# Kernel optimization log

Measured on AMD Instinct MI355X. Metric: run time of the kernel, lower is better.

The kernel has to match this reference:

```python
import jax, jax.numpy as jnp
import numpy as np
import math


def setup_inputs() -> dict:
    key = jax.random.key(0)
    k1, k2, k3 = jax.random.split(key, 3)
    B, H, T, D = 4, 16, 4096, 128
    return {
        "q": jax.random.normal(k1, (B, H, T, D), dtype=jnp.float32),
        "k": jax.random.normal(k2, (B, H, T, D), dtype=jnp.float32),
        "v": jax.random.normal(k3, (B, H, T, D), dtype=jnp.float32),
        "BS": 32,
    }


def _compress(x, block_size):
    # blockwise mean-pool along T: [B,H,T,D] -> [B,H,C,D], C = ceil(T/BS)
    B, H, T, D = x.shape
    C = math.ceil(T / block_size)
    pad = C * block_size - T
    if pad:
        x = jnp.pad(x, ((0, 0), (0, 0), (0, pad), (0, 0)))
    return x.reshape(B, H, C, block_size, D).mean(axis=3)


def reference(q, k, v, BS):
    dk = k.shape[-1]
    k_cmp = _compress(k, BS)  # [B,H,C,D]
    v_cmp = _compress(v, BS)  # [B,H,C,D]
    # scaled dot-product attention over compressed KV
    score = jnp.einsum("bhtd,bhcd->bhtc", q, k_cmp) / math.sqrt(dk)
    score = jax.nn.softmax(score, axis=-1)  # [B,H,T,C]
    out = jnp.einsum("bhtc,bhcd->bhtd", score, v_cmp)  # [B,H,T,D]
    return (out, score)
```

## Files before the change

kernel.cpp:

```cpp
#include <hip/hip_runtime.h>
#include <hip/hip_bf16.h>

typedef __attribute__((ext_vector_type(8))) short short8;
typedef __attribute__((ext_vector_type(4))) float f32x4;

#define B_  4
#define H_  16
#define T_  4096
#define D_  128
#define BS_ 32
#define C_  128
#define BH_ (B_ * H_)

__device__ __forceinline__ int posperm(int x) {
  return (x & ~31) | (((x >> 2) & 3) << 3) | (((x >> 4) & 1) << 2) | (x & 3);
}

__device__ __forceinline__ unsigned short f2bf(float f) {
  __hip_bfloat16 h = __float2bfloat16(f);
  return __builtin_bit_cast(unsigned short, h);
}

__device__ __forceinline__ void gload_lds16(const uint4* g, uint4* l) {
  __builtin_amdgcn_global_load_lds(
      (const __attribute__((address_space(1))) unsigned int*)g,
      (__attribute__((address_space(3))) unsigned int*)l, 16, 0, 0);
}

__global__ __launch_bounds__(256) void compress_kernel(
    const float* __restrict__ k, const float* __restrict__ v,
    unsigned short* __restrict__ kc, unsigned short* __restrict__ vT) {
  int blk = blockIdx.x;
  int bh  = blk >> 4;
  int cg  = blk & 15;
  int cb  = cg * 8 + (threadIdx.x >> 5);
  int l   = threadIdx.x & 31;
  const float* kp = k + ((size_t)bh * T_ + (size_t)cb * BS_) * D_ + 4 * l;
  const float* vp = v + ((size_t)bh * T_ + (size_t)cb * BS_) * D_ + 4 * l;
  float4 ks = {0.f, 0.f, 0.f, 0.f}, vs = {0.f, 0.f, 0.f, 0.f};
#pragma unroll
  for (int j = 0; j < BS_; ++j) {
    float4 a = *(const float4*)(kp + (size_t)j * D_);
    float4 b = *(const float4*)(vp + (size_t)j * D_);
    ks.x += a.x; ks.y += a.y; ks.z += a.z; ks.w += a.w;
    vs.x += b.x; vs.y += b.y; vs.z += b.z; vs.w += b.w;
  }
  const float s = 1.0f / BS_;
  size_t slab = (size_t)bh * (C_ * D_);
  unsigned short kq[4] = {f2bf(ks.x * s), f2bf(ks.y * s), f2bf(ks.z * s), f2bf(ks.w * s)};
  int p0 = posperm(4 * l) ^ ((cb & 7) << 3);
  *(uint2*)&kc[slab + (size_t)cb * D_ + p0] = *(const uint2*)kq;
  float vv[4] = {vs.x * s, vs.y * s, vs.z * s, vs.w * s};
#pragma unroll
  for (int i = 0; i < 4; ++i) {
    int d = 4 * l + i;
    vT[slab + (size_t)d * C_ + (posperm(cb) ^ ((d & 7) << 3))] = f2bf(vv[i]);
  }
}

__global__ __launch_bounds__(256, 4) void attn_kernel(
    const float* __restrict__ q, const unsigned short* __restrict__ kc,
    const unsigned short* __restrict__ vT, float* __restrict__ out,
    float* __restrict__ score) {
  __shared__ uint4 sbuf[2048];

  int blk    = blockIdx.x;
  int bh     = blk >> 6;
  int tchunk = blk & 63;
  int tid    = threadIdx.x;
  int wave   = tid >> 6;
  int lane   = tid & 63;
  int g      = lane >> 4;
  int lr     = lane & 15;
  int rx     = lr & 7;
  int t0     = tchunk * 64 + wave * 16;

  const uint4* kg = (const uint4*)(kc + (size_t)bh * (C_ * D_));
  const uint4* vg = (const uint4*)(vT + (size_t)bh * (C_ * D_));
#pragma unroll
  for (int it = 0; it < 8; ++it) {
    gload_lds16(&kg[it * 256 + tid], &sbuf[it * 256 + tid]);
  }

  const float scale = 0.08838834764831845f;
  short8 qf[4];
  const float* qrow = q + ((size_t)bh * T_ + t0 + lr) * D_;
#pragma unroll
  for (int ks = 0; ks < 4; ++ks) {
    int d0 = 4 * g + 32 * ks;
    float4 a = *(const float4*)(qrow + d0);
    float4 b = *(const float4*)(qrow + d0 + 16);
    short8 f;
    f[0] = (short)f2bf(a.x * scale); f[1] = (short)f2bf(a.y * scale);
    f[2] = (short)f2bf(a.z * scale); f[3] = (short)f2bf(a.w * scale);
    f[4] = (short)f2bf(b.x * scale); f[5] = (short)f2bf(b.y * scale);
    f[6] = (short)f2bf(b.z * scale); f[7] = (short)f2bf(b.w * scale);
    qf[ks] = f;
  }
  __syncthreads();

  f32x4 accS[8];
#pragma unroll
  for (int cm = 0; cm < 8; ++cm) accS[cm] = f32x4{0.f, 0.f, 0.f, 0.f};
#pragma unroll
  for (int cm = 0; cm < 8; ++cm) {
    int rbase = (lr + 16 * cm) * 16;
#pragma unroll
    for (int ks = 0; ks < 4; ++ks) {
      uint4 kf = sbuf[rbase + ((4 * ks + g) ^ rx)];
      accS[cm] = __builtin_amdgcn_mfma_f32_16x16x32_bf16(
          __builtin_bit_cast(short8, kf), qf[ks], accS[cm], 0, 0, 0);
    }
  }

  float m = -3.0e38f;
#pragma unroll
  for (int cm = 0; cm < 8; ++cm)
#pragma unroll
    for (int r = 0; r < 4; ++r) m = fmaxf(m, accS[cm][r]);
  m = fmaxf(m, __shfl_xor(m, 16));
  m = fmaxf(m, __shfl_xor(m, 32));

  float sum = 0.f;
#pragma unroll
  for (int cm = 0; cm < 8; ++cm) {
#pragma unroll
    for (int r = 0; r < 4; ++r) {
      float p = __expf(accS[cm][r] - m);
      accS[cm][r] = p;
      sum += p;
    }
  }
  sum += __shfl_xor(sum, 16);
  sum += __shfl_xor(sum, 32);
  float inv = 1.0f / sum;
#pragma unroll
  for (int cm = 0; cm < 8; ++cm)
#pragma unroll
    for (int r = 0; r < 4; ++r) accS[cm][r] *= inv;

  __syncthreads();

  float* bw = (float*)sbuf + wave * 2048;
#pragma unroll
  for (int cm = 0; cm < 8; ++cm) {
    int c4 = (g + 4 * cm) ^ rx;
    *(f32x4*)&bw[lr * 128 + c4 * 4] = accS[cm];
  }
  float* dstS = score + ((size_t)bh * T_ + t0) * C_;
#pragma unroll
  for (int j = 0; j < 8; ++j) {
    int row = 2 * j + (lane >> 5);
    int c4  = lane & 31;
    f32x4 val = *(const f32x4*)&bw[row * 128 + (c4 ^ (row & 7)) * 4];
    *(f32x4*)&dstS[(size_t)row * C_ + c4 * 4] = val;
  }

  short8 pf[4];
#pragma unroll
  for (int ks = 0; ks < 4; ++ks) {
    short8 f;
#pragma unroll
    for (int r = 0; r < 4; ++r) {
      f[r]     = (short)f2bf(accS[2 * ks][r]);
      f[4 + r] = (short)f2bf(accS[2 * ks + 1][r]);
    }
    pf[ks] = f;
  }

#pragma unroll
  for (int nt = 0; nt < 8; ++nt) {
    f32x4 o = f32x4{0.f, 0.f, 0.f, 0.f};
    int rbase = (lr + 16 * nt) * 16;
#pragma unroll
    for (int ks = 0; ks < 4; ++ks) {
      uint4 vf = vg[rbase + ((4 * ks + g) ^ rx)];
      o = __builtin_amdgcn_mfma_f32_16x16x32_bf16(
          __builtin_bit_cast(short8, vf), pf[ks], o, 0, 0, 0);
    }
    int c4 = (g + 4 * nt) ^ rx;
    *(f32x4*)&bw[lr * 128 + c4 * 4] = o;
  }
  float* dstO = out + ((size_t)bh * T_ + t0) * D_;
#pragma unroll
  for (int j = 0; j < 8; ++j) {
    int row = 2 * j + (lane >> 5);
    int c4  = lane & 31;
    f32x4 val = *(const f32x4*)&bw[row * 128 + (c4 ^ (row & 7)) * 4];
    *(f32x4*)&dstO[(size_t)row * D_ + c4 * 4] = val;
  }
}

extern "C" void kernel_launch(void* const* d_in, const int* in_sizes, int n_in,
                              void* d_out, int out_size, void* d_ws, size_t ws_size,
                              hipStream_t stream) {
  const float* q = (const float*)d_in[0];
  const float* k = (const float*)d_in[1];
  const float* v = (const float*)d_in[2];
  float* out   = (float*)d_out;
  float* score = out + (size_t)BH_ * T_ * D_;

  unsigned short* kc = (unsigned short*)d_ws;
  unsigned short* vT = kc + (size_t)BH_ * C_ * D_;

  compress_kernel<<<BH_ * 16, 256, 0, stream>>>(k, v, kc, vT);
  attn_kernel<<<BH_ * 64, 256, 0, stream>>>(q, kc, vT, out, score);
}
```

Baseline: 152.5 us.

## Stage V tile in LDS, fold softmax scale into K, nontemporal output stores

Moves the 1/sqrt(d) scale into the compress kernel so Q only needs conversion, issues Q global loads before the K LDS prefetch, and loads the compressed V tile into shared memory with async global-to-LDS copies instead of reading it from global memory per MFMA. Score and output writes become nontemporal stores to avoid polluting cache. The change adds extra barriers and an LDS round trip for V, and folding the scale before bf16 rounding slightly changes numerics.

```diff
diff --git a/kernel.cpp b/kernel.cpp
--- a/kernel.cpp
+++ b/kernel.cpp
@@ -45,9 +45,10 @@
     ks.x += a.x; ks.y += a.y; ks.z += a.z; ks.w += a.w;
     vs.x += b.x; vs.y += b.y; vs.z += b.z; vs.w += b.w;
   }
-  const float s = 1.0f / BS_;
+  const float s  = 1.0f / BS_;
+  const float sk = s * 0.08838834764831845f;
   size_t slab = (size_t)bh * (C_ * D_);
-  unsigned short kq[4] = {f2bf(ks.x * s), f2bf(ks.y * s), f2bf(ks.z * s), f2bf(ks.w * s)};
+  unsigned short kq[4] = {f2bf(ks.x * sk), f2bf(ks.y * sk), f2bf(ks.z * sk), f2bf(ks.w * sk)};
   int p0 = posperm(4 * l) ^ ((cb & 7) << 3);
   *(uint2*)&kc[slab + (size_t)cb * D_ + p0] = *(const uint2*)kq;
   float vv[4] = {vs.x * s, vs.y * s, vs.z * s, vs.w * s};
@@ -77,24 +78,27 @@
 
   const uint4* kg = (const uint4*)(kc + (size_t)bh * (C_ * D_));
   const uint4* vg = (const uint4*)(vT + (size_t)bh * (C_ * D_));
-#pragma unroll
-  for (int it = 0; it < 8; ++it) {
-    gload_lds16(&kg[it * 256 + tid], &sbuf[it * 256 + tid]);
-  }
-
-  const float scale = 0.08838834764831845f;
-  short8 qf[4];
+
   const float* qrow = q + ((size_t)bh * T_ + t0 + lr) * D_;
+  float4 qa[4], qb[4];
 #pragma unroll
   for (int ks = 0; ks < 4; ++ks) {
     int d0 = 4 * g + 32 * ks;
-    float4 a = *(const float4*)(qrow + d0);
-    float4 b = *(const float4*)(qrow + d0 + 16);
+    qa[ks] = *(const float4*)(qrow + d0);
+    qb[ks] = *(const float4*)(qrow + d0 + 16);
+  }
+
+#pragma unroll
+  for (int it = 0; it < 8; ++it) gload_lds16(&kg[it * 256 + tid], &sbuf[it * 256 + tid]);
+
+  short8 qf[4];
+#pragma unroll
+  for (int ks = 0; ks < 4; ++ks) {
     short8 f;
-    f[0] = (short)f2bf(a.x * scale); f[1] = (short)f2bf(a.y * scale);
-    f[2] = (short)f2bf(a.z * scale); f[3] = (short)f2bf(a.w * scale);
-    f[4] = (short)f2bf(b.x * scale); f[5] = (short)f2bf(b.y * scale);
-    f[6] = (short)f2bf(b.z * scale); f[7] = (short)f2bf(b.w * scale);
+    f[0] = (short)f2bf(qa[ks].x); f[1] = (short)f2bf(qa[ks].y);
+    f[2] = (short)f2bf(qa[ks].z); f[3] = (short)f2bf(qa[ks].w);
+    f[4] = (short)f2bf(qb[ks].x); f[5] = (short)f2bf(qb[ks].y);
+    f[6] = (short)f2bf(qb[ks].z); f[7] = (short)f2bf(qb[ks].w);
     qf[ks] = f;
   }
   __syncthreads();
@@ -153,7 +157,7 @@
     int row = 2 * j + (lane >> 5);
     int c4  = lane & 31;
     f32x4 val = *(const f32x4*)&bw[row * 128 + (c4 ^ (row & 7)) * 4];
-    *(f32x4*)&dstS[(size_t)row * C_ + c4 * 4] = val;
+    __builtin_nontemporal_store(val, (f32x4*)&dstS[(size_t)row * C_ + c4 * 4]);
   }
 
   short8 pf[4];
@@ -167,19 +171,31 @@
     }
     pf[ks] = f;
   }
-
+  __syncthreads();
+
+#pragma unroll
+  for (int it = 0; it < 8; ++it) gload_lds16(&vg[it * 256 + tid], &sbuf[it * 256 + tid]);
+  __syncthreads();
+
+  f32x4 o[8];
+#pragma unroll
+  for (int nt = 0; nt < 8; ++nt) o[nt] = f32x4{0.f, 0.f, 0.f, 0.f};
 #pragma unroll
   for (int nt = 0; nt < 8; ++nt) {
-    f32x4 o = f32x4{0.f, 0.f, 0.f, 0.f};
     int rbase = (lr + 16 * nt) * 16;
 #pragma unroll
     for (int ks = 0; ks < 4; ++ks) {
-      uint4 vf = vg[rbase + ((4 * ks + g) ^ rx)];
-      o = __builtin_amdgcn_mfma_f32_16x16x32_bf16(
-          __builtin_bit_cast(short8, vf), pf[ks], o, 0, 0, 0);
-    }
+      uint4 vf = sbuf[rbase + ((4 * ks + g) ^ rx)];
+      o[nt] = __builtin_amdgcn_mfma_f32_16x16x32_bf16(
+          __builtin_bit_cast(short8, vf), pf[ks], o[nt], 0, 0, 0);
+    }
+  }
+  __syncthreads();
+
+#pragma unroll
+  for (int nt = 0; nt < 8; ++nt) {
     int c4 = (g + 4 * nt) ^ rx;
-    *(f32x4*)&bw[lr * 128 + c4 * 4] = o;
+    *(f32x4*)&bw[lr * 128 + c4 * 4] = o[nt];
   }
   float* dstO = out + ((size_t)bh * T_ + t0) * D_;
 #pragma unroll
@@ -187,7 +203,7 @@
     int row = 2 * j + (lane >> 5);
     int c4  = lane & 31;
     f32x4 val = *(const f32x4*)&bw[row * 128 + (c4 ^ (row & 7)) * 4];
-    *(f32x4*)&dstO[(size_t)row * D_ + c4 * 4] = val;
+    __builtin_nontemporal_store(val, (f32x4*)&dstO[(size_t)row * D_ + c4 * 4]);
   }
 }
 
```

After: 128.0 us. 1.19x faster.
